# Performance work log

Hardware: AMD Instinct MI355X
Metric: run time of the kernel (lower is better)

Reference implementation:

```python
import jax, jax.numpy as jnp
import numpy as np

Q, N, D = 4096, 100000, 128


def setup_inputs() -> dict:
    key = jax.random.key(0)
    k1, k2, k3 = jax.random.split(key, 3)
    inputs = jax.random.normal(k1, (Q, D), dtype=jnp.float32)
    X_train = jax.random.normal(k2, (N, D), dtype=jnp.float32)
    y_train = jax.random.normal(k3, (N,), dtype=jnp.float32)
    return {"inputs": inputs, "X_train": X_train, "y_train": y_train, "k": 32}


def reference(inputs, X_train, y_train, k):
    # Squared Euclidean distances [Q, N] via the expanded identity
    # |a-b|^2 = |a|^2 + |b|^2 - 2 a.b  (avoids materializing [Q, N, D]).
    q_sq = jnp.sum(inputs * inputs, axis=-1, keepdims=True)        # [Q, 1]
    t_sq = jnp.sum(X_train * X_train, axis=-1)                     # [N]
    cross = jnp.einsum('qd,nd->qn', inputs, X_train)               # [Q, N]
    distances = q_sq + t_sq[None, :] - 2.0 * cross                 # [Q, N]
    # top_k of -distances == k nearest neighbors
    _, indices = jax.lax.top_k(-distances, k)                      # [Q, k]
    nearest = y_train[indices]                                     # [Q, k]
    return jnp.mean(nearest, axis=1)                               # [Q]
```

## Files before the change

kernel.cpp:

```cpp
#include <hip/hip_runtime.h>
#include <hip/hip_fp16.h>
#include <cstdint>
#include <cstddef>


constexpr int Q_  = 4096;
constexpr int N_  = 100000;
constexpr int D_  = 128;
constexpr int K_  = 32;

constexpr int QT    = 32;
constexpr int BN    = 256;
constexpr int NCH   = 8;
constexpr int NSUB  = 16;
constexpr int CHUNK = 12544;
constexpr int HALF0 = 6400;
constexpr int NPAD  = NCH * CHUNK;
constexpr int CWS   = 64;
constexpr int QTS   = 16;
constexpr int SAMP_M      = 8192;
constexpr int SAMP_STRIDE = 12;
constexpr int SAMP_OFF    = 5;
constexpr int SAMP_ITERS  = SAMP_M / BN;

constexpr int XS_B  = NPAD / 64;
constexpr int SAM_B = SAMP_M / 64;
constexpr int PQ_B  = Q_ / 4;
constexpr int MXN   = XS_B * 4;

typedef __attribute__((ext_vector_type(8))) _Float16 half8;
typedef __attribute__((ext_vector_type(4))) float    floatx4;
typedef unsigned long long ull;

#define DEV __device__ __forceinline__
constexpr ull DEADC = ~0ull;

DEV ull pack_cand(float score, unsigned int n) {
    unsigned int s = __float_as_uint(score);
    s = (s & 0x80000000u) ? ~s : (s | 0x80000000u);
    return ((ull)s << 32) | (ull)n;
}
DEV float unpack_score(ull k) {
    unsigned int s = (unsigned int)(k >> 32);
    s = (s & 0x80000000u) ? (s ^ 0x80000000u) : ~s;
    return __uint_as_float(s);
}
DEV ull u64min(ull a, ull b) { return a < b ? a : b; }
DEV float inf_f() { return __int_as_float(0x7f800000); }

DEV ull bitonic64(ull v, int L) {
    #pragma unroll
    for (int k2 = 2; k2 <= 64; k2 <<= 1)
        #pragma unroll
        for (int j2 = k2 >> 1; j2 >= 1; j2 >>= 1) {
            ull o = __shfl_xor(v, j2);
            bool up = ((L & k2) == 0);
            bool lo = ((L & j2) == 0);
            ull mn = u64min(v, o), mx = v ^ o ^ mn;
            v = (lo == up) ? mn : mx;
        }
    return v;
}
DEV ull bimerge64(ull v, int L) {
    #pragma unroll
    for (int j2 = 32; j2 >= 1; j2 >>= 1) {
        ull o = __shfl_xor(v, j2);
        ull mn = u64min(v, o), mx = v ^ o ^ mn;
        v = ((L & j2) == 0) ? mn : mx;
    }
    return v;
}

__global__ void prep_all(const float* __restrict__ X, const float* __restrict__ Qm,
                         __half* __restrict__ Xs, float* __restrict__ tsq,
                         float* __restrict__ mxArr, float* __restrict__ mxArrH,
                         __half* __restrict__ Xsam, float* __restrict__ tsqS,
                         __half* __restrict__ Qh,
                         float* __restrict__ qsq, float* __restrict__ qrs,
                         int* __restrict__ flagF)
{
    const int tid = threadIdx.x, L = tid & 63, wv = tid >> 6;
    const int bx = blockIdx.x;
    const int am = L & 15, aq = L >> 4;

    if (bx < XS_B) {
        int t16 = bx * 4 + wv;
        int r = t16 * 16 + am;
        float ssq = 0.f, xr2 = 0.f, xh2 = 0.f;
        #pragma unroll
        for (int ks = 0; ks < 4; ++ks) {
            int c = ks * 32 + aq * 8;
            float v0=0,v1=0,v2=0,v3=0,v4=0,v5=0,v6=0,v7=0;
            if (r < N_) {
                float4 a = *(const float4*)(X + (size_t)r * D_ + c);
                float4 b = *(const float4*)(X + (size_t)r * D_ + c + 4);
                v0=a.x; v1=a.y; v2=a.z; v3=a.w; v4=b.x; v5=b.y; v6=b.z; v7=b.w;
            }
            half8 h;
            h[0]=(_Float16)v0; h[1]=(_Float16)v1; h[2]=(_Float16)v2; h[3]=(_Float16)v3;
            h[4]=(_Float16)v4; h[5]=(_Float16)v5; h[6]=(_Float16)v6; h[7]=(_Float16)v7;
            float c0=(float)h[0], c1=(float)h[1], c2=(float)h[2], c3=(float)h[3];
            float c4=(float)h[4], c5=(float)h[5], c6=(float)h[6], c7=(float)h[7];
            float r0=v0-c0, r1=v1-c1, r2=v2-c2, r3=v3-c3;
            float r4=v4-c4, r5=v5-c5, r6=v6-c6, r7=v7-c7;
            ssq += v0*v0+v1*v1+v2*v2+v3*v3+v4*v4+v5*v5+v6*v6+v7*v7;
            xr2 += r0*r0+r1*r1+r2*r2+r3*r3+r4*r4+r5*r5+r6*r6+r7*r7;
            xh2 += c0*c0+c1*c1+c2*c2+c3*c3+c4*c4+c5*c5+c6*c6+c7*c7;
            *(half8*)(Xs + ((size_t)(t16 * 4 + ks)) * 512 + L * 8) = h;
        }
        ssq += __shfl_xor(ssq, 16); ssq += __shfl_xor(ssq, 32);
        xr2 += __shfl_xor(xr2, 16); xr2 += __shfl_xor(xr2, 32);
        xh2 += __shfl_xor(xh2, 16); xh2 += __shfl_xor(xh2, 32);
        if (aq == 0) tsq[r] = (r < N_) ? ssq : inf_f();
        float m = xr2;
        m = fmaxf(m, __shfl_xor(m, 1)); m = fmaxf(m, __shfl_xor(m, 2));
        m = fmaxf(m, __shfl_xor(m, 4)); m = fmaxf(m, __shfl_xor(m, 8));
        float mh = xh2;
        mh = fmaxf(mh, __shfl_xor(mh, 1)); mh = fmaxf(mh, __shfl_xor(mh, 2));
        mh = fmaxf(mh, __shfl_xor(mh, 4)); mh = fmaxf(mh, __shfl_xor(mh, 8));
        if (L == 0) { mxArr[t16] = m; mxArrH[t16] = mh; }
    } else if (bx < XS_B + SAM_B) {
        int t16 = (bx - XS_B) * 4 + wv;
        int j = t16 * 16 + am;
        int n = j * SAMP_STRIDE + SAMP_OFF;
        float ssq = 0.f;
        #pragma unroll
        for (int ks = 0; ks < 4; ++ks) {
            int c = ks * 32 + aq * 8;
            float4 a = *(const float4*)(X + (size_t)n * D_ + c);
            float4 b = *(const float4*)(X + (size_t)n * D_ + c + 4);
            half8 h;
            h[0]=(_Float16)a.x; h[1]=(_Float16)a.y; h[2]=(_Float16)a.z; h[3]=(_Float16)a.w;
            h[4]=(_Float16)b.x; h[5]=(_Float16)b.y; h[6]=(_Float16)b.z; h[7]=(_Float16)b.w;
            ssq += a.x*a.x + a.y*a.y + a.z*a.z + a.w*a.w
                 + b.x*b.x + b.y*b.y + b.z*b.z + b.w*b.w;
            *(half8*)(Xsam + ((size_t)(t16 * 4 + ks)) * 512 + L * 8) = h;
        }
        ssq += __shfl_xor(ssq, 16); ssq += __shfl_xor(ssq, 32);
        if (aq == 0) tsqS[j] = ssq;
    } else {
        int r = (bx - XS_B - SAM_B) * 4 + wv;
        float2 x = *(const float2*)(Qm + (size_t)r * D_ + 2 * L);
        __half h0 = __float2half(x.x), h1 = __float2half(x.y);
        size_t o = (size_t)r * D_ + 2 * L;
        Qh[o] = h0; Qh[o + 1] = h1;
        float r0 = x.x - __half2float(h0), r1 = x.y - __half2float(h1);
        float s  = x.x * x.x + x.y * x.y;
        float sr = r0 * r0 + r1 * r1;
        s  += __shfl_xor(s, 32);  s += __shfl_xor(s, 16);  s += __shfl_xor(s, 8);
        s  += __shfl_xor(s, 4);   s += __shfl_xor(s, 2);   s += __shfl_xor(s, 1);
        sr += __shfl_xor(sr, 32); sr += __shfl_xor(sr, 16); sr += __shfl_xor(sr, 8);
        sr += __shfl_xor(sr, 4);  sr += __shfl_xor(sr, 2);  sr += __shfl_xor(sr, 1);
        if (L == 0) { qsq[r] = s; qrs[r] = sr; flagF[r] = 0; }
    }
}

__global__ void reduce_mx(const float* __restrict__ mxArr,
                          const float* __restrict__ mxArrH,
                          float* __restrict__ mxOut)
{
    __shared__ float sR[4], sH[4];
    const int tid = threadIdx.x, L = tid & 63, wv = tid >> 6;
    float a = 0.f, b = 0.f;
    #pragma unroll 1
    for (int i = tid; i < MXN; i += 256) {
        a = fmaxf(a, mxArr[i]);
        b = fmaxf(b, mxArrH[i]);
    }
    #pragma unroll
    for (int s = 32; s; s >>= 1) {
        a = fmaxf(a, __shfl_xor(a, s));
        b = fmaxf(b, __shfl_xor(b, s));
    }
    if (L == 0) { sR[wv] = a; sH[wv] = b; }
    __syncthreads();
    if (tid == 0) {
        mxOut[0] = fmaxf(fmaxf(sR[0], sR[1]), fmaxf(sR[2], sR[3]));
        mxOut[1] = fmaxf(fmaxf(sH[0], sH[1]), fmaxf(sH[2], sH[3]));
    }
}

__global__ __launch_bounds__(256, 2) void sample_T(
    const __half* __restrict__ Qh, const __half* __restrict__ Xsam,
    const float* __restrict__ tsqS, const float* __restrict__ qsq,
    const float* __restrict__ qrs, const float* __restrict__ mxOut,
    float* __restrict__ Teff, float* __restrict__ rawT, float* __restrict__ EwA)
{
    __shared__ float sT[QTS][130];
    const int tid = threadIdx.x, L = tid & 63, wv = tid >> 6;
    const int qbase = blockIdx.x * QTS;
    const int nwv = wv * 64;
    const int am = L & 15, aq = L >> 4;

    half8 afh[4];
    #pragma unroll
    for (int ks = 0; ks < 4; ++ks) {
        size_t o = (size_t)(qbase + am) * D_ + ks * 32 + aq * 8;
        afh[ks] = *(const half8*)(Qh + o);
    }

    float t2a[4], t2b[4];
    #pragma unroll
    for (int rg = 0; rg < 4; ++rg) { t2a[rg] = inf_f(); t2b[rg] = inf_f(); }

    const __half* bp = Xsam + (size_t)nwv * 128 + (size_t)L * 8;
    const float*  tp = tsqS + nwv + am;

    half8 bc[4], bn[4];
    #pragma unroll
    for (int nt = 0; nt < 4; ++nt)
        bc[nt] = *(const half8*)(bp + nt * 2048);

    #pragma unroll 1
    for (int it = 0; it < SAMP_ITERS; ++it) {
        float ts[4];
        #pragma unroll
        for (int nt = 0; nt < 4; ++nt) ts[nt] = tp[nt * 16];

        floatx4 acc[4] = {};
        #pragma unroll
        for (int ks = 0; ks < 4; ++ks) {
            const __half* pp = (ks < 3) ? (bp + (ks + 1) * 512) : (bp + 32768);
            #pragma unroll
            for (int nt = 0; nt < 4; ++nt)
                bn[nt] = *(const half8*)(pp + nt * 2048);
            #pragma unroll
            for (int nt = 0; nt < 4; ++nt)
                acc[nt] = __builtin_amdgcn_mfma_f32_16x16x32_f16(
                    afh[ks], bc[nt], acc[nt], 0, 0, 0);
            #pragma unroll
            for (int nt = 0; nt < 4; ++nt) bc[nt] = bn[nt];
        }
        #pragma unroll
        for (int rg = 0; rg < 4; ++rg) {
            float m1 = t2a[rg], m2 = t2b[rg];
            #pragma unroll
            for (int nt = 0; nt < 4; ++nt) {
                float v = ts[nt] - 2.f * acc[nt][rg];
                if (v < m2) { if (v < m1) { m2 = m1; m1 = v; } else m2 = v; }
            }
            t2a[rg] = m1; t2b[rg] = m2;
        }
        bp += 32768; tp += BN;
    }
    #pragma unroll
    for (int rg = 0; rg < 4; ++rg) {
        int q = aq * 4 + rg;
        sT[q][wv * 32 + am * 2 + 0] = t2a[rg];
        sT[q][wv * 32 + am * 2 + 1] = t2b[rg];
    }
    __syncthreads();

    const float mxr = mxOut[0], mxh = mxOut[1];

    #pragma unroll 1
    for (int j = 0; j < 4; ++j) {
        int q = wv * 4 + j;
        float a = sT[q][2 * L], b = sT[q][2 * L + 1];
        float g = 0.f;
        #pragma unroll 1
        for (int r = 0; r < 16; ++r) {
            float mn = fminf(a, b);
            mn = fminf(mn, __shfl_xor(mn, 32)); mn = fminf(mn, __shfl_xor(mn, 16));
            mn = fminf(mn, __shfl_xor(mn, 8));  mn = fminf(mn, __shfl_xor(mn, 4));
            mn = fminf(mn, __shfl_xor(mn, 2));  mn = fminf(mn, __shfl_xor(mn, 1));
            g = mn;
            ull ba = __ballot(a == g);
            if (ba) { if (L == __ffsll(ba) - 1) a = inf_f(); }
            else    { ull bb = __ballot(b == g); if (L == __ffsll(bb) - 1) b = inf_f(); }
        }
        if (L == 0) {
            int gq = qbase + q;
            float e = 2.f * (sqrtf(qsq[gq]) * sqrtf(mxr)
                           + sqrtf(qrs[gq]) * sqrtf(mxh)) + 0.02f;
            rawT[gq] = g; EwA[gq] = e; Teff[gq] = g + e;
        }
    }
}

__global__ __launch_bounds__(256, 2) void knn_main(
    const __half* __restrict__ Qh, const __half* __restrict__ Xs,
    const float* __restrict__ tsq, const float* __restrict__ Teff,
    ull* __restrict__ candG, int* __restrict__ cntC, int* __restrict__ flagF)
{
    __shared__ ull candL[QT][CWS];
    __shared__ int cntL[QT];

    const int tid = threadIdx.x, L = tid & 63, wv = tid >> 6;
    const int lb = blockIdx.x, ch = lb & 7;
    const int half = (lb >> 3) & 1, sub = lb & 15;
    const int qbase = (lb >> 4) * QT, nwv = wv * 64;
    const int rowBase = ch * CHUNK + half * HALF0;
    const int iters = half ? 24 : 25;
    const int am = L & 15, aq = L >> 4;

    if (tid < QT) cntL[tid] = 0;
    __syncthreads();

    float th[2][4];
    float nH[2];
    #pragma unroll
    for (int qt = 0; qt < 2; ++qt) {
        #pragma unroll
        for (int rg = 0; rg < 4; ++rg)
            th[qt][rg] = Teff[qbase + qt * 16 + aq * 4 + rg];
        float m = fmaxf(fmaxf(th[qt][0], th[qt][1]), fmaxf(th[qt][2], th[qt][3]));
        nH[qt] = -0.5f * m - 1e-3f;
    }

    half8 afh[2][4];
    #pragma unroll
    for (int qt = 0; qt < 2; ++qt)
        #pragma unroll
        for (int ks = 0; ks < 4; ++ks) {
            size_t o = (size_t)(qbase + qt * 16 + am) * D_ + ks * 32 + aq * 8;
            afh[qt][ks] = *(const half8*)(Qh + o);
        }

    const __half* bp = Xs + (size_t)(rowBase + nwv) * 128 + (size_t)L * 8;
    const float*  tp = tsq + rowBase + nwv + am;
    int n0 = rowBase + nwv + am;

    half8 bx[8], by[8];
    #pragma unroll
    for (int j = 0; j < 8; ++j)
        bx[j] = *(const half8*)(bp + (j >> 2) * 512 + (j & 3) * 2048);

    #pragma unroll 1
    for (int it = 0; it < iters; ++it) {
        float ts[4];
        #pragma unroll
        for (int nt = 0; nt < 4; ++nt) ts[nt] = tp[nt * 16];

        floatx4 acc[2][4] = {};

        #pragma unroll
        for (int j = 0; j < 8; ++j)
            by[j] = *(const half8*)(bp + (2 + (j >> 2)) * 512 + (j & 3) * 2048);
        #pragma unroll
        for (int ks = 0; ks < 2; ++ks)
            #pragma unroll
            for (int nt = 0; nt < 4; ++nt) {
                acc[0][nt] = __builtin_amdgcn_mfma_f32_16x16x32_f16(
                    afh[0][ks], bx[ks * 4 + nt], acc[0][nt], 0, 0, 0);
                acc[1][nt] = __builtin_amdgcn_mfma_f32_16x16x32_f16(
                    afh[1][ks], bx[ks * 4 + nt], acc[1][nt], 0, 0, 0);
            }

        #pragma unroll
        for (int j = 0; j < 8; ++j)
            bx[j] = *(const half8*)(bp + 32768 + (j >> 2) * 512 + (j & 3) * 2048);
        #pragma unroll
        for (int ks = 0; ks < 2; ++ks)
            #pragma unroll
            for (int nt = 0; nt < 4; ++nt) {
                acc[0][nt] = __builtin_amdgcn_mfma_f32_16x16x32_f16(
                    afh[0][2 + ks], by[ks * 4 + nt], acc[0][nt], 0, 0, 0);
                acc[1][nt] = __builtin_amdgcn_mfma_f32_16x16x32_f16(
                    afh[1][2 + ks], by[ks * 4 + nt], acc[1][nt], 0, 0, 0);
            }

        unsigned hit = 0;
        #pragma unroll
        for (int nt = 0; nt < 4; ++nt) {
            #pragma unroll
            for (int qt = 0; qt < 2; ++qt) {
                float mx = fmaxf(fmaxf(acc[qt][nt][0], acc[qt][nt][1]),
                                 fmaxf(acc[qt][nt][2], acc[qt][nt][3]));
                float Gm = fmaf(0.5f, ts[nt], nH[qt]);
                if (mx > Gm) hit |= 1u << (nt * 2 + qt);
            }
        }
        if (__any(hit != 0)) {
            #pragma unroll
            for (int nt = 0; nt < 4; ++nt) {
                #pragma unroll
                for (int qt = 0; qt < 2; ++qt) {
                    if (!__any(hit & (1u << (nt * 2 + qt)))) continue;
                    unsigned n = (unsigned)(n0 + nt * 16);
                    #pragma unroll
                    for (int rg = 0; rg < 4; ++rg) {
                        float s = fmaf(-2.f, acc[qt][nt][rg], ts[nt]);
                        if (s < th[qt][rg]) {
                            int q = qt * 16 + aq * 4 + rg;
                            int pos = atomicAdd(&cntL[q], 1);
                            if (pos < CWS)
                                candL[q][pos] = pack_cand(s, n);
                            else
                                flagF[qbase + q] = 1;
                        }
                    }
                }
            }
        }
        bp += 32768; tp += BN; n0 += BN;
    }

    __syncthreads();

    #pragma unroll 1
    for (int j = 0; j < 8; ++j) {
        int q = wv * 8 + j;
        int gq = qbase + q;
        int c = cntL[q];
        int cc = c < CWS ? c : CWS;
        ull* dst = candG + ((size_t)gq * NSUB + sub) * CWS;
        if (L < cc) dst[L] = candL[q][L];
        if (L == 0) cntC[gq * NSUB + sub] = cc;
    }
}

__global__ void finalize(const ull* __restrict__ candG, const int* __restrict__ cntC,
                         const int* __restrict__ flagF, const float* __restrict__ Qm,
                         const float* __restrict__ X, const float* __restrict__ tsq,
                         const float* __restrict__ rawT, const float* __restrict__ EwA,
                         const float* __restrict__ Ytr, float* __restrict__ out)
{
    __shared__ ull fb[4][256];
    int L = threadIdx.x & 63;
    int wv = threadIdx.x >> 6;
    int q = blockIdx.x * 4 + wv;
    bool bad = (flagF[q] != 0);
    float result = 0.f;

    if (!bad) {
        int cg = (L < NSUB) ? cntC[q * NSUB + L] : 0;
        int ctot = cg;
        ctot += __shfl_xor(ctot, 32); ctot += __shfl_xor(ctot, 16);
        ctot += __shfl_xor(ctot, 8);  ctot += __shfl_xor(ctot, 4);
        ctot += __shfl_xor(ctot, 2);  ctot += __shfl_xor(ctot, 1);
        if (ctot < K_) bad = true;
        else {
            ull s = DEADC;
            #pragma unroll 1
            for (int g = 0; g < NSUB; ++g) {
                int c_g = __shfl(cg, g);
                if (c_g == 0) continue;
                const ull* cb = candG + ((size_t)q * NSUB + g) * CWS;
                ull v = (L < c_g) ? cb[L] : DEADC;
                v = bitonic64(v, L);
                ull w = __shfl(v, 63 - L);
                s = bimerge64(u64min(s, w), L);
            }
            int cr = ctot < 64 ? ctot : 64;
            unsigned n = (unsigned)(s & 0xffffffffu);
            ull pe = DEADC;
            if (L < cr) {
                const float4* xp = (const float4*)(X + (size_t)n * D_);
                const float4* qp = (const float4*)(Qm + (size_t)q * D_);
                float d = 0.f;
                #pragma unroll 8
                for (int i = 0; i < 32; ++i) {
                    float4 xv = xp[i], qv = qp[i];
                    d += qv.x * xv.x + qv.y * xv.y + qv.z * xv.z + qv.w * xv.w;
                }
                pe = pack_cand(tsq[n] - 2.f * d, n);
            }
            ull pe2 = bitonic64(pe, L);
            float exact31 = unpack_score(__shfl(pe2, K_ - 1));
            bool ok = exact31 < rawT[q];
            if (ctot > 64) {
                float A63 = unpack_score(__shfl(s, 63));
                ok = ok && (A63 - EwA[q] > exact31);
            }
            if (!ok) bad = true;
            else {
                float ys = 0.f;
                if (L < K_) ys = Ytr[(unsigned)(pe2 & 0xffffffffu)];
                ys += __shfl_xor(ys, 32); ys += __shfl_xor(ys, 16);
                ys += __shfl_xor(ys, 8);  ys += __shfl_xor(ys, 4);
                ys += __shfl_xor(ys, 2);  ys += __shfl_xor(ys, 1);
                result = ys * (1.f / K_);
            }
        }
    }

    if (bad) {
        const float4* qp = (const float4*)(Qm + (size_t)q * D_);
        float T = rawT[q] + EwA[q];
        float lo = 0.f, hi = 0.f;
        bool haveLo = false, haveHi = false;
        int cnt = 0;
        #pragma unroll 1
        for (int att = 0; att < 40; ++att) {
            cnt = 0;
            #pragma unroll 1
            for (int j = 0; j < NPAD / 64; ++j) {
                int n = j * 64 + L;
                float s = inf_f();
                if (n < N_) {
                    const float4* xp = (const float4*)(X + (size_t)n * D_);
                    float d = 0.f;
                    #pragma unroll 4
                    for (int i = 0; i < 32; ++i) {
                        float4 xv = xp[i], qv = qp[i];
                        d += qv.x * xv.x + qv.y * xv.y + qv.z * xv.z + qv.w * xv.w;
                    }
                    s = tsq[n] - 2.f * d;
                }
                bool want = s < T;
                ull m = __ballot(want);
                if (m) {
                    int pos = cnt + (int)__popcll(m & ((1ull << L) - 1ull));
                    if (want && pos < 256) fb[wv][pos] = pack_cand(s, (unsigned)n);
                    cnt += (int)__popcll(m);
                }
            }
            if (cnt >= K_ && cnt <= 256) break;
            if (cnt < K_) { lo = T; haveLo = true;
                T = haveHi ? 0.5f * (T + hi) : T + exp2f((float)att) * 0.5f; }
            else { hi = T; haveHi = true;
                T = haveLo ? 0.5f * (lo + T) : T - exp2f((float)att) * 0.5f; }
        }
        if (cnt >= K_ && cnt <= 256) {
            ull s64 = DEADC;
            #pragma unroll 1
            for (int off = 0; off < 256; off += 64) {
                if (off >= cnt) break;
                ull v = (off + L < cnt) ? fb[wv][off + L] : DEADC;
                v = bitonic64(v, L);
                ull w = __shfl(v, 63 - L);
                s64 = bimerge64(u64min(s64, w), L);
            }
            float ys = (L < K_) ? Ytr[(unsigned)(s64 & 0xffffffffu)] : 0.f;
            ys += __shfl_xor(ys, 32); ys += __shfl_xor(ys, 16);
            ys += __shfl_xor(ys, 8);  ys += __shfl_xor(ys, 4);
            ys += __shfl_xor(ys, 2);  ys += __shfl_xor(ys, 1);
            result = ys * (1.f / K_);
        } else {
            ull last = 0;
            float ysum = 0.f;
            for (int r = 0; r < K_; ++r) {
                ull best = DEADC;
                for (int j = 0; j < NPAD / 64; ++j) {
                    int n = j * 64 + L;
                    if (n < N_) {
                        const float4* xp = (const float4*)(X + (size_t)n * D_);
                        float d = 0.f;
                        #pragma unroll 4
                        for (int i = 0; i < 32; ++i) {
                            float4 xv = xp[i], qv = qp[i];
                            d += qv.x * xv.x + qv.y * xv.y + qv.z * xv.z + qv.w * xv.w;
                        }
                        ull k = pack_cand(tsq[n] - 2.f * d, n);
                        if (k > last && k < best) best = k;
                    }
                }
                best = u64min(best, __shfl_xor(best, 32));
                best = u64min(best, __shfl_xor(best, 16));
                best = u64min(best, __shfl_xor(best, 8));
                best = u64min(best, __shfl_xor(best, 4));
                best = u64min(best, __shfl_xor(best, 2));
                best = u64min(best, __shfl_xor(best, 1));
                if (L == 0) ysum += Ytr[(unsigned)(best & 0xffffffffu)];
                last = best;
            }
            result = ysum * (1.f / K_);
        }
    }
    if (L == 0) out[q] = result;
}

extern "C" void kernel_launch(void* const* d_in, const int* in_sizes, int n_in,
                              void* d_out, int out_size, void* d_ws, size_t ws_size,
                              hipStream_t stream)
{
    const float* Qm  = (const float*)d_in[0];
    const float* X   = (const float*)d_in[1];
    const float* Ytr = (const float*)d_in[2];
    float* out = (float*)d_out;

    char* w = (char*)d_ws;
    auto alloc = [&](size_t bytes) {
        char* p = w; w += (bytes + 255) & ~(size_t)255; return p;
    };
    __half* Xs   = (__half*)  alloc((size_t)(NPAD + BN) * D_ * 2);
    __half* Qh   = (__half*)  alloc((size_t)Q_ * D_ * 2);
    float*  ts   = (float*)   alloc((size_t)NPAD * 4);
    __half* Xsm  = (__half*)  alloc((size_t)(SAMP_M + BN) * D_ * 2);
    float*  tsS  = (float*)   alloc((size_t)SAMP_M * 4);
    ull*    cd   = (ull*)     alloc((size_t)Q_ * NSUB * CWS * 8);
    int*    cnC  = (int*)     alloc((size_t)Q_ * NSUB * 4);
    int*    flg  = (int*)     alloc((size_t)Q_ * 4);
    float*  mxA  = (float*)   alloc((size_t)MXN * 4);
    float*  mxAH = (float*)   alloc((size_t)MXN * 4);
    float*  mxO  = (float*)   alloc(256);
    float*  Tef  = (float*)   alloc((size_t)Q_ * 4);
    float*  rwT  = (float*)   alloc((size_t)Q_ * 4);
    float*  Ew   = (float*)   alloc((size_t)Q_ * 4);
    float*  qs   = (float*)   alloc((size_t)Q_ * 4);
    float*  qr2  = (float*)   alloc((size_t)Q_ * 4);

    prep_all<<<XS_B + SAM_B + PQ_B, 256, 0, stream>>>(
        X, Qm, Xs, ts, mxA, mxAH, Xsm, tsS, Qh, qs, qr2, flg);
    reduce_mx<<<1, 256, 0, stream>>>(mxA, mxAH, mxO);
    sample_T<<<Q_ / QTS, 256, 0, stream>>>(Qh, Xsm, tsS, qs, qr2, mxO,
                                           Tef, rwT, Ew);
    knn_main<<<(Q_ / QT) * NSUB, 256, 0, stream>>>(Qh, Xs, ts, Tef, cd, cnC, flg);
    finalize<<<Q_ / 4, 256, 0, stream>>>(cd, cnC, flg, Qm, X, ts, rwT, Ew, Ytr, out);
}
```

Baseline: 400.6 us.

## Double query tile per block to reuse train fragments across four query tiles

Raises the per-block query tile from 32 to 64, so each wave runs MFMAs for four 16-query tiles against every loaded train-row fragment. This halves the global/L2 traffic for the training set per query. The B-fragment loads become a rolling per-k-step prefetch, with the next iteration's first fragment loaded during the last k-step. Launch bounds drop to one block per SIMD group because accumulators and A fragments double in register use, which lowers occupancy and the ability to hide latency.

New measurement: 547.8 us. 36.8% more time.

```diff
diff --git a/kernel.cpp b/kernel.cpp
--- a/kernel.cpp
+++ b/kernel.cpp
@@ -9,7 +9,7 @@
 constexpr int D_  = 128;
 constexpr int K_  = 32;
 
-constexpr int QT    = 32;
+constexpr int QT    = 64;
 constexpr int BN    = 256;
 constexpr int NCH   = 8;
 constexpr int NSUB  = 16;
@@ -278,7 +278,7 @@
     }
 }
 
-__global__ __launch_bounds__(256, 2) void knn_main(
+__global__ __launch_bounds__(256, 1) void knn_main(
     const __half* __restrict__ Qh, const __half* __restrict__ Xs,
     const float* __restrict__ tsq, const float* __restrict__ Teff,
     ull* __restrict__ candG, int* __restrict__ cntC, int* __restrict__ flagF)
@@ -297,10 +297,10 @@
     if (tid < QT) cntL[tid] = 0;
     __syncthreads();
 
-    float th[2][4];
-    float nH[2];
-    #pragma unroll
-    for (int qt = 0; qt < 2; ++qt) {
+    float th[4][4];
+    float nH[4];
+    #pragma unroll
+    for (int qt = 0; qt < 4; ++qt) {
         #pragma unroll
         for (int rg = 0; rg < 4; ++rg)
             th[qt][rg] = Teff[qbase + qt * 16 + aq * 4 + rg];
@@ -308,9 +308,9 @@
         nH[qt] = -0.5f * m - 1e-3f;
     }
 
-    half8 afh[2][4];
-    #pragma unroll
-    for (int qt = 0; qt < 2; ++qt)
+    half8 afh[4][4];
+    #pragma unroll
+    for (int qt = 0; qt < 4; ++qt)
         #pragma unroll
         for (int ks = 0; ks < 4; ++ks) {
             size_t o = (size_t)(qbase + qt * 16 + am) * D_ + ks * 32 + aq * 8;
@@ -321,10 +321,10 @@
     const float*  tp = tsq + rowBase + nwv + am;
     int n0 = rowBase + nwv + am;
 
-    half8 bx[8], by[8];
-    #pragma unroll
-    for (int j = 0; j < 8; ++j)
-        bx[j] = *(const half8*)(bp + (j >> 2) * 512 + (j & 3) * 2048);
+    half8 bc[4], bn[4];
+    #pragma unroll
+    for (int nt = 0; nt < 4; ++nt)
+        bc[nt] = *(const half8*)(bp + nt * 2048);
 
     #pragma unroll 1
     for (int it = 0; it < iters; ++it) {
@@ -332,51 +332,41 @@
         #pragma unroll
         for (int nt = 0; nt < 4; ++nt) ts[nt] = tp[nt * 16];
 
-        floatx4 acc[2][4] = {};
-
-        #pragma unroll
-        for (int j = 0; j < 8; ++j)
-            by[j] = *(const half8*)(bp + (2 + (j >> 2)) * 512 + (j & 3) * 2048);
-        #pragma unroll
-        for (int ks = 0; ks < 2; ++ks)
+        floatx4 acc[4][4] = {};
+        #pragma unroll
+        for (int ks = 0; ks < 4; ++ks) {
+            const __half* pp = (ks < 3) ? (bp + (ks + 1) * 512) : (bp + 32768);
+            #pragma unroll
+            for (int nt = 0; nt < 4; ++nt)
+                bn[nt] = *(const half8*)(pp + nt * 2048);
             #pragma unroll
             for (int nt = 0; nt < 4; ++nt) {
-                acc[0][nt] = __builtin_amdgcn_mfma_f32_16x16x32_f16(
-                    afh[0][ks], bx[ks * 4 + nt], acc[0][nt], 0, 0, 0);
-                acc[1][nt] = __builtin_amdgcn_mfma_f32_16x16x32_f16(
-                    afh[1][ks], bx[ks * 4 + nt], acc[1][nt], 0, 0, 0);
-            }
-
-        #pragma unroll
-        for (int j = 0; j < 8; ++j)
-            bx[j] = *(const half8*)(bp + 32768 + (j >> 2) * 512 + (j & 3) * 2048);
-        #pragma unroll
-        for (int ks = 0; ks < 2; ++ks)
-            #pragma unroll
-            for (int nt = 0; nt < 4; ++nt) {
-                acc[0][nt] = __builtin_amdgcn_mfma_f32_16x16x32_f16(
-                    afh[0][2 + ks], by[ks * 4 + nt], acc[0][nt], 0, 0, 0);
-                acc[1][nt] = __builtin_amdgcn_mfma_f32_16x16x32_f16(
-                    afh[1][2 + ks], by[ks * 4 + nt], acc[1][nt], 0, 0, 0);
-            }
+                #pragma unroll
+                for (int qt = 0; qt < 4; ++qt)
+                    acc[qt][nt] = __builtin_amdgcn_mfma_f32_16x16x32_f16(
+                        afh[qt][ks], bc[nt], acc[qt][nt], 0, 0, 0);
+            }
+            #pragma unroll
+            for (int nt = 0; nt < 4; ++nt) bc[nt] = bn[nt];
+        }
 
         unsigned hit = 0;
         #pragma unroll
         for (int nt = 0; nt < 4; ++nt) {
             #pragma unroll
-            for (int qt = 0; qt < 2; ++qt) {
+            for (int qt = 0; qt < 4; ++qt) {
                 float mx = fmaxf(fmaxf(acc[qt][nt][0], acc[qt][nt][1]),
                                  fmaxf(acc[qt][nt][2], acc[qt][nt][3]));
                 float Gm = fmaf(0.5f, ts[nt], nH[qt]);
-                if (mx > Gm) hit |= 1u << (nt * 2 + qt);
+                if (mx > Gm) hit |= 1u << (nt * 4 + qt);
             }
         }
         if (__any(hit != 0)) {
             #pragma unroll
             for (int nt = 0; nt < 4; ++nt) {
                 #pragma unroll
-                for (int qt = 0; qt < 2; ++qt) {
-                    if (!__any(hit & (1u << (nt * 2 + qt)))) continue;
+                for (int qt = 0; qt < 4; ++qt) {
+                    if (!__any(hit & (1u << (nt * 4 + qt)))) continue;
                     unsigned n = (unsigned)(n0 + nt * 16);
                     #pragma unroll
                     for (int rg = 0; rg < 4; ++rg) {
@@ -399,8 +389,8 @@
     __syncthreads();
 
     #pragma unroll 1
-    for (int j = 0; j < 8; ++j) {
-        int q = wv * 8 + j;
+    for (int j = 0; j < 16; ++j) {
+        int q = wv * 16 + j;
         int gq = qbase + q;
         int c = cntL[q];
         int cc = c < CWS ? c : CWS;
```
